# Kernel tuning notes

Measured on AMD Instinct MI355X. Metric: run time of the kernel, lower is better.

The kernel has to match this reference:

```python
import jax, jax.numpy as jnp
import numpy as np

SH_DIM = 9                      # (sh_deg+1)^2, sh_deg=2
DATA_DIM = SH_DIM * 3 + 1       # 28
FINE = 8
COARSE = 32
RADIUS = 1.3
NUM_ATOMS = 16
BATCH = 128
STEP = (RADIUS * 2.0 / COARSE / FINE) / 2.0   # fine_voxel_len / 2
N_INTRS = COARSE * 3 * 2 * FINE               # 1536


def sh_encode(dirs):
    # degree-2 real spherical harmonics bases, [.., 9]
    x, y, z = dirs[..., 0], dirs[..., 1], dirs[..., 2]
    C0 = 0.28209479177387814
    C1 = 0.4886025119029199
    C2 = (1.0925484305920792, -1.0925484305920792, 0.31539156525252005,
          -1.0925484305920792, 0.5462742152960396)
    return jnp.stack([
        jnp.full_like(x, C0), -C1 * y, C1 * z, -C1 * x,
        C2[0] * x * y, C2[1] * y * z, C2[2] * (2.0 * z * z - x * x - y * y),
        C2[3] * x * z, C2[4] * (x * x - y * y)], axis=-1)


def dict_interp(grid, atoms, pts):
    # pts: [N,3] normalized to [0,1). grid: [COARSE^3, A]. atoms: [FINE^3, A, D].
    # coarse voxel -> dictionary coefficients; trilinear interp of atoms inside it.
    cpos = pts * COARSE
    cidx = jnp.clip(jnp.floor(cpos), 0, COARSE - 1)
    ci = cidx.astype(jnp.int32)
    coeff = grid[(ci[:, 0] * COARSE + ci[:, 1]) * COARSE + ci[:, 2]]  # [N, A]
    local = cpos - cidx                       # [0,1) within coarse voxel
    fpos = local * FINE - 0.5
    f0f = jnp.floor(fpos)
    w = fpos - f0f                            # trilinear weights
    f0 = f0f.astype(jnp.int32)
    out = jnp.zeros((pts.shape[0], DATA_DIM), dtype=pts.dtype)
    for dx in (0, 1):
        for dy in (0, 1):
            for dz in (0, 1):
                ix = jnp.clip(f0[:, 0] + dx, 0, FINE - 1)
                iy = jnp.clip(f0[:, 1] + dy, 0, FINE - 1)
                iz = jnp.clip(f0[:, 2] + dz, 0, FINE - 1)
                wt = ((w[:, 0] if dx else 1.0 - w[:, 0]) *
                      (w[:, 1] if dy else 1.0 - w[:, 1]) *
                      (w[:, 2] if dz else 1.0 - w[:, 2]))
                vals = jnp.einsum('na,nad->nd', coeff, atoms[(ix * FINE + iy) * FINE + iz])
                out = out + wt[:, None] * vals
    return out


def setup_inputs() -> dict:
    key = jax.random.key(0)
    k1, k2, k3, k4 = jax.random.split(key, 4)
    rays_o = jnp.array([0.0, 0.0, -2.0 * RADIUS]) + 0.05 * jax.random.normal(k1, (BATCH, 3), jnp.float32)
    d = 0.25 * jax.random.normal(k2, (BATCH, 3), jnp.float32) + jnp.array([0.0, 0.0, 1.0])
    rays_d = d / jnp.linalg.norm(d, axis=-1, keepdims=True)
    grid = 0.01 * jax.random.normal(k3, (COARSE ** 3, NUM_ATOMS), jnp.float32)
    atoms_sh = jax.random.uniform(k4, (FINE ** 3, NUM_ATOMS, DATA_DIM - 1), jnp.float32)
    atoms = jnp.concatenate([atoms_sh, jnp.full((FINE ** 3, NUM_ATOMS, 1), 0.01, jnp.float32)], -1)
    return {"rays_o": rays_o, "rays_d": rays_d, "grid": grid, "atoms": atoms, "grid_id": 0}


def reference(rays_o, rays_d, grid, atoms, grid_id):
    B = rays_o.shape[0]
    # ---- sample_proposal (no-grad in original) ----
    off_pos = (RADIUS - rays_o) / rays_d
    off_neg = (-RADIUS - rays_o) / rays_d
    start = jnp.max(jnp.minimum(off_pos, off_neg), axis=-1, keepdims=True)
    steps = jnp.arange(N_INTRS, dtype=rays_o.dtype)[None, :]
    intersections = jax.lax.stop_gradient(start + steps * STEP)        # [B, 1536]
    tsec = intersections[:, :-1]                                       # [B, M]
    M = N_INTRS - 1
    pts = rays_o[:, None, :] + tsec[:, :, None] * rays_d[:, None, :]   # [B, M, 3]
    mask = jnp.all((pts > -RADIUS) & (pts < RADIUS), axis=-1)          # [B, M]
    pts_n = jnp.clip((pts + RADIUS) / (2.0 * RADIUS), 0.0, 1.0 - 1e-6)
    pts_n = jax.lax.stop_gradient(pts_n).reshape(-1, 3)
    # ---- dictionary interpolation (computed densely, zeroed by mask) ----
    data = dict_interp(grid, atoms, pts_n).reshape(B, M, DATA_DIM)
    sigma = jax.nn.relu(jnp.where(mask, data[..., -1], 0.0))           # [B, M]
    # ---- sigma -> alpha / weights ----
    dists = (intersections[:, 1:] - intersections[:, :-1]) * jnp.linalg.norm(rays_d, axis=-1, keepdims=True)
    alpha = 1.0 - jnp.exp(-sigma * dists)
    trans = jnp.concatenate([jnp.ones((B, 1), alpha.dtype),
                             jnp.cumprod(1.0 - alpha + 1e-10, axis=-1)[:, :-1]], axis=-1)
    abs_light = alpha * trans                                          # [B, M]
    # ---- SH -> rgb, composite ----
    sh_mult = sh_encode(rays_d)[:, None, None, :]                      # [B,1,1,9]
    sh = data[..., :-1].reshape(B, M, 3, SH_DIM)
    rgb_raw = jnp.where(mask[..., None], jnp.sum(sh_mult * sh, axis=-1), 0.0)  # [B,M,3]
    rgb = jnp.sum(abs_light[..., None] * jax.nn.sigmoid(rgb_raw), axis=1)
    rgb = rgb + (1.0 - jnp.sum(abs_light, axis=-1))[:, None]           # white background
    depth = jnp.sum(abs_light * tsec, axis=-1)
    return rgb, alpha, depth
```

## Files before the change

kernel.cpp:

```cpp
#include <hip/hip_runtime.h>
#include <hip/hip_fp16.h>

typedef unsigned int u32;
typedef _Float16 half2v __attribute__((ext_vector_type(2)));
union H2 { u32 u; half2v v; };

#define MSAMP 1535
#define NS 1024
#define RADF 1.3f
#define STEPF ((float)(1.3 * 2.0 / 32.0 / 8.0 / 2.0))

__global__ __launch_bounds__(256) void k_t(const float* __restrict__ atoms,
                                           __half* __restrict__ wst) {
    int o = blockIdx.x * 256 + threadIdx.x;
    int s = o >> 15;
    int r = o & 32767;
    int cell = r >> 6;
    int j = (r >> 4) & 3;
    int a = r & 15;
    wst[o] = __float2half(atoms[(cell * 16 + a) * 28 + s * 4 + j]);
}

__global__ __launch_bounds__(512) void k_p1(const float* __restrict__ ro,
                                            const float* __restrict__ rd,
                                            const float* __restrict__ gridf,
                                            const __half* __restrict__ wst,
                                            __half* __restrict__ raw) {
    __shared__ __half hl[512 * 68];
    int bx = blockIdx.x;
    int s   = bx >> 7;
    int ray = bx & 127;
    int tid = threadIdx.x;

    {
        const uint2* src = (const uint2*)(wst + s * 32768);
#pragma unroll
        for (int it = 0; it < 16; it++) {
            int idx = it * 512 + tid;
            uint2 v = src[idx];
            int cell  = idx >> 4;
            int inner = (idx & 15) << 2;
            *(uint2*)&hl[cell * 68 + inner] = v;
        }
    }
    __syncthreads();

    float ox = ro[ray * 3 + 0], oy = ro[ray * 3 + 1], oz = ro[ray * 3 + 2];
    float dx = rd[ray * 3 + 0], dy = rd[ray * 3 + 1], dz = rd[ray * 3 + 2];
    float a0 = ( RADF - ox) / dx, b0 = (-RADF - ox) / dx;
    float a1 = ( RADF - oy) / dy, b1 = (-RADF - oy) / dy;
    float a2 = ( RADF - oz) / dz, b2 = (-RADF - oz) / dz;
    float st = fmaxf(fmaxf(fminf(a0, b0), fminf(a1, b1)), fminf(a2, b2));

    for (int m = tid; m < NS; m += 512) {
        float t = st + (float)m * STEPF;
        float px = ox + t * dx, py = oy + t * dy, pz = oz + t * dz;
        bool inb = (px > -RADF) && (px < RADF) && (py > -RADF) && (py < RADF)
                && (pz > -RADF) && (pz < RADF);
        if (!inb) continue;

        const float inv2R = 1.0f / 2.6f;
        float pnx = fminf(fmaxf((px + RADF) * inv2R, 0.0f), 0.999999f);
        float pny = fminf(fmaxf((py + RADF) * inv2R, 0.0f), 0.999999f);
        float pnz = fminf(fmaxf((pz + RADF) * inv2R, 0.0f), 0.999999f);

        float cpx = pnx * 32.0f, cpy = pny * 32.0f, cpz = pnz * 32.0f;
        float cfx = floorf(cpx), cfy = floorf(cpy), cfz = floorf(cpz);
        int cix = (int)cfx, ciy = (int)cfy, ciz = (int)cfz;

        float fpx = (cpx - cfx) * 8.0f - 0.5f;
        float fpy = (cpy - cfy) * 8.0f - 0.5f;
        float fpz = (cpz - cfz) * 8.0f - 0.5f;
        float ffx = floorf(fpx), ffy = floorf(fpy), ffz = floorf(fpz);
        int f0x = (int)ffx, f0y = (int)ffy, f0z = (int)ffz;
        float wx = fpx - ffx, wy = fpy - ffy, wz = fpz - ffz;

        int ixa[2] = { max(f0x, 0), min(f0x + 1, 7) };
        int iya[2] = { max(f0y, 0), min(f0y + 1, 7) };
        int iza[2] = { max(f0z, 0), min(f0z + 1, 7) };
        float wxa[2] = { 1.0f - wx, wx };
        float wya[2] = { 1.0f - wy, wy };
        float wza[2] = { 1.0f - wz, wz };

        half2v ch[8];
        {
            const float4* cp = (const float4*)(gridf + (((cix * 32 + ciy) * 32 + ciz) << 4));
            float4 c0 = cp[0], c1 = cp[1], c2 = cp[2], c3 = cp[3];
            ch[0] = half2v{(_Float16)c0.x, (_Float16)c0.y};
            ch[1] = half2v{(_Float16)c0.z, (_Float16)c0.w};
            ch[2] = half2v{(_Float16)c1.x, (_Float16)c1.y};
            ch[3] = half2v{(_Float16)c1.z, (_Float16)c1.w};
            ch[4] = half2v{(_Float16)c2.x, (_Float16)c2.y};
            ch[5] = half2v{(_Float16)c2.z, (_Float16)c2.w};
            ch[6] = half2v{(_Float16)c3.x, (_Float16)c3.y};
            ch[7] = half2v{(_Float16)c3.z, (_Float16)c3.w};
        }

        float acc[4] = {0.0f, 0.0f, 0.0f, 0.0f};

#pragma unroll
        for (int cx = 0; cx < 2; cx++)
#pragma unroll
        for (int cy = 0; cy < 2; cy++)
#pragma unroll
        for (int cz = 0; cz < 2; cz++) {
            float wt = wxa[cx] * wya[cy] * wza[cz];
            int cb = ((ixa[cx] * 8 + iya[cy]) * 8 + iza[cz]) * 68;
            float dd[4] = {0.0f, 0.0f, 0.0f, 0.0f};
#pragma unroll
            for (int g = 0; g < 4; g++) {
#pragma unroll
                for (int j = 0; j < 4; j++) {
                    uint2 q = *(const uint2*)&hl[cb + j * 16 + g * 4];
                    H2 a0h, a1h; a0h.u = q.x; a1h.u = q.y;
                    dd[j] = __builtin_amdgcn_fdot2(a0h.v, ch[2 * g],     dd[j], false);
                    dd[j] = __builtin_amdgcn_fdot2(a1h.v, ch[2 * g + 1], dd[j], false);
                }
            }
#pragma unroll
            for (int j = 0; j < 4; j++) acc[j] = fmaf(wt, dd[j], acc[j]);
        }

        __half2 p0 = __floats2half2_rn(acc[0], acc[1]);
        __half2 p1 = __floats2half2_rn(acc[2], acc[3]);
        uint2 pv;
        pv.x = *(u32*)&p0;
        pv.y = *(u32*)&p1;
        *(uint2*)&raw[(ray * NS + m) * 28 + s * 4] = pv;
    }
}

__global__ __launch_bounds__(512) void k_p2(const float* __restrict__ ro,
                                            const float* __restrict__ rd,
                                            const __half* __restrict__ raw,
                                            float* __restrict__ rgb_out,
                                            float* __restrict__ alpha_out,
                                            float* __restrict__ depth_out) {
    int ray = blockIdx.x;
    int t = threadIdx.x;
    int lane = t & 63, wave = t >> 6;

    int abase = ray * MSAMP;
    for (int m = NS + t; m < MSAMP; m += 512) alpha_out[abase + m] = 0.0f;

    float ox = ro[ray * 3 + 0], oy = ro[ray * 3 + 1], oz = ro[ray * 3 + 2];
    float dx = rd[ray * 3 + 0], dy = rd[ray * 3 + 1], dz = rd[ray * 3 + 2];
    float a0 = ( RADF - ox) / dx, b0 = (-RADF - ox) / dx;
    float a1 = ( RADF - oy) / dy, b1 = (-RADF - oy) / dy;
    float a2 = ( RADF - oz) / dz, b2 = (-RADF - oz) / dz;
    float st = fmaxf(fmaxf(fminf(a0, b0), fminf(a1, b1)), fminf(a2, b2));
    float nrm = sqrtf(dx * dx + dy * dy + dz * dz);

    float shm[9];
    shm[0] = 0.28209479177387814f;
    shm[1] = -0.4886025119029199f * dy;
    shm[2] =  0.4886025119029199f * dz;
    shm[3] = -0.4886025119029199f * dx;
    shm[4] =  1.0925484305920792f * dx * dy;
    shm[5] = -1.0925484305920792f * dy * dz;
    shm[6] =  0.31539156525252005f * (2.0f * dz * dz - dx * dx - dy * dy);
    shm[7] = -1.0925484305920792f * dx * dz;
    shm[8] =  0.5462742152960396f * (dx * dx - dy * dy);

    float av[2], sr[2], sg[2], sb[2];
#pragma unroll
    for (int k = 0; k < 2; k++) {
        int m = t * 2 + k;
        float tm = st + (float)m * STEPF;
        float px = ox + tm * dx, py = oy + tm * dy, pz = oz + tm * dz;
        bool inb = (px > -RADF) && (px < RADF) && (py > -RADF) && (py < RADF)
                && (pz > -RADF) && (pz < RADF);
        float alpha = 0.0f, r0 = 0.0f, r1 = 0.0f, r2 = 0.0f;
        if (inb) {
            const __half* rp = raw + (ray * NS + m) * 28;
            float v[28];
#pragma unroll
            for (int i = 0; i < 7; i++) {
                uint2 q = *(const uint2*)(rp + i * 4);
                __half2 h0 = *(__half2*)&q.x;
                __half2 h1 = *(__half2*)&q.y;
                float2 f0v = __half22float2(h0);
                float2 f1v = __half22float2(h1);
                v[i*4+0] = f0v.x; v[i*4+1] = f0v.y; v[i*4+2] = f1v.x; v[i*4+3] = f1v.y;
            }
            float sigma = fmaxf(v[27], 0.0f);
            alpha = 1.0f - __expf(-sigma * STEPF * nrm);
            float rr[3];
#pragma unroll
            for (int cch = 0; cch < 3; cch++) {
                float sdot = 0.0f;
#pragma unroll
                for (int j = 0; j < 9; j++) sdot = fmaf(shm[j], v[cch * 9 + j], sdot);
                rr[cch] = 1.0f / (1.0f + __expf(-sdot));
            }
            r0 = rr[0]; r1 = rr[1]; r2 = rr[2];
        }
        av[k] = alpha; sr[k] = r0; sg[k] = r1; sb[k] = r2;
        alpha_out[abase + m] = alpha;
    }

    float p = (1.0f - av[0] + 1e-10f) * (1.0f - av[1] + 1e-10f);

    float incl = p;
#pragma unroll
    for (int off = 1; off < 64; off <<= 1) {
        float vv = __shfl_up(incl, off);
        if (lane >= off) incl *= vv;
    }
    __shared__ float wprod[8];
    if (lane == 63) wprod[wave] = incl;
    __syncthreads();
    float excl = __shfl_up(incl, 1);
    if (lane == 0) excl = 1.0f;
    for (int w = 0; w < 8; w++) if (w < wave) excl *= wprod[w];

    float trans = excl;
    float ra = 0.0f, ga = 0.0f, ba = 0.0f, da = 0.0f, wsum = 0.0f;
#pragma unroll
    for (int k = 0; k < 2; k++) {
        int m = t * 2 + k;
        float al = av[k];
        float w = al * trans;
        ra = fmaf(w, sr[k], ra);
        ga = fmaf(w, sg[k], ga);
        ba = fmaf(w, sb[k], ba);
        da = fmaf(w, st + (float)m * STEPF, da);
        wsum += w;
        trans *= (1.0f - al + 1e-10f);
    }

    float vals[5] = { ra, ga, ba, da, wsum };
    __shared__ float wred[8][5];
#pragma unroll
    for (int i = 0; i < 5; i++) {
        float v = vals[i];
        v += __shfl_xor(v, 1);  v += __shfl_xor(v, 2);  v += __shfl_xor(v, 4);
        v += __shfl_xor(v, 8);  v += __shfl_xor(v, 16); v += __shfl_xor(v, 32);
        if (lane == 0) wred[wave][i] = v;
    }
    __syncthreads();
    if (t == 0) {
        float res[5];
#pragma unroll
        for (int i = 0; i < 5; i++) {
            float r_ = 0.0f;
            for (int w = 0; w < 8; w++) r_ += wred[w][i];
            res[i] = r_;
        }
        float omw = 1.0f - res[4];
        rgb_out[ray * 3 + 0] = res[0] + omw;
        rgb_out[ray * 3 + 1] = res[1] + omw;
        rgb_out[ray * 3 + 2] = res[2] + omw;
        depth_out[ray] = res[3];
    }
}

extern "C" void kernel_launch(void* const* d_in, const int* in_sizes, int n_in,
                              void* d_out, int out_size, void* d_ws, size_t ws_size,
                              hipStream_t stream) {
    const float* ro    = (const float*)d_in[0];
    const float* rd    = (const float*)d_in[1];
    const float* grid  = (const float*)d_in[2];
    const float* atoms = (const float*)d_in[3];
    int B = in_sizes[0] / 3;

    __half* wst = (__half*)d_ws;
    __half* raw = (__half*)((char*)d_ws + 458752);

    float* out       = (float*)d_out;
    float* rgb_out   = out;
    float* alpha_out = out + B * 3;
    float* depth_out = out + B * 3 + B * MSAMP;

    hipLaunchKernelGGL(k_t,  dim3(896), dim3(256), 0, stream, atoms, wst);
    hipLaunchKernelGGL(k_p1, dim3(896), dim3(512), 0, stream, ro, rd, grid, wst, raw);
    hipLaunchKernelGGL(k_p2, dim3(B),   dim3(512), 0, stream, ro, rd, raw,
                       rgb_out, alpha_out, depth_out);
}
```

Before: 86.89 us.

## Pack two rays per block in k_p1 and give k_p2 one sample per thread

k_t now reads atoms coalesced and scatters the transposed fp16 writes, instead of gathering strided reads. k_p1 handles two rays per block, so each 64KB shared atom slice is loaded half as often across the grid, and the fill uses 16-byte loads. k_p2 moves to 1024 threads with one sample per thread, which removes the per-thread serial pair and widens the scan to 16 waves. The costs are half as many k_p1 blocks and a larger block for k_p2, which could hurt occupancy or latency hiding.

```diff
diff --git a/kernel.cpp b/kernel.cpp
--- a/kernel.cpp
+++ b/kernel.cpp
@@ -13,12 +13,13 @@
 __global__ __launch_bounds__(256) void k_t(const float* __restrict__ atoms,
                                            __half* __restrict__ wst) {
     int o = blockIdx.x * 256 + threadIdx.x;
-    int s = o >> 15;
-    int r = o & 32767;
-    int cell = r >> 6;
-    int j = (r >> 4) & 3;
-    int a = r & 15;
-    wst[o] = __float2half(atoms[(cell * 16 + a) * 28 + s * 4 + j]);
+    float v = atoms[o];
+    int cell = o / 448;
+    int r = o - cell * 448;
+    int a = r / 28;
+    int d = r - a * 28;
+    int s = d >> 2, j = d & 3;
+    wst[s * 32768 + cell * 64 + j * 16 + a] = __float2half(v);
 }
 
 __global__ __launch_bounds__(512) void k_p1(const float* __restrict__ ro,
@@ -28,19 +29,22 @@
                                             __half* __restrict__ raw) {
     __shared__ __half hl[512 * 68];
     int bx = blockIdx.x;
-    int s   = bx >> 7;
-    int ray = bx & 127;
+    int s  = bx >> 6;
+    int pr = bx & 63;
     int tid = threadIdx.x;
+    int ray = pr * 2 + (tid >> 8);
+    int q   = tid & 255;
 
     {
-        const uint2* src = (const uint2*)(wst + s * 32768);
-#pragma unroll
-        for (int it = 0; it < 16; it++) {
+        const uint4* src = (const uint4*)(wst + s * 32768);
+#pragma unroll
+        for (int it = 0; it < 8; it++) {
             int idx = it * 512 + tid;
-            uint2 v = src[idx];
-            int cell  = idx >> 4;
-            int inner = (idx & 15) << 2;
-            *(uint2*)&hl[cell * 68 + inner] = v;
+            uint4 v = src[idx];
+            int cell  = idx >> 3;
+            int inner = (idx & 7) << 3;
+            *(uint2*)&hl[cell * 68 + inner]     = make_uint2(v.x, v.y);
+            *(uint2*)&hl[cell * 68 + inner + 4] = make_uint2(v.z, v.w);
         }
     }
     __syncthreads();
@@ -52,7 +56,9 @@
     float a2 = ( RADF - oz) / dz, b2 = (-RADF - oz) / dz;
     float st = fmaxf(fmaxf(fminf(a0, b0), fminf(a1, b1)), fminf(a2, b2));
 
-    for (int m = tid; m < NS; m += 512) {
+#pragma unroll
+    for (int k = 0; k < 4; k++) {
+        int m = q + k * 256;
         float t = st + (float)m * STEPF;
         float px = ox + t * dx, py = oy + t * dy, pz = oz + t * dz;
         bool inb = (px > -RADF) && (px < RADF) && (py > -RADF) && (py < RADF)
@@ -111,8 +117,8 @@
             for (int g = 0; g < 4; g++) {
 #pragma unroll
                 for (int j = 0; j < 4; j++) {
-                    uint2 q = *(const uint2*)&hl[cb + j * 16 + g * 4];
-                    H2 a0h, a1h; a0h.u = q.x; a1h.u = q.y;
+                    uint2 qv = *(const uint2*)&hl[cb + j * 16 + g * 4];
+                    H2 a0h, a1h; a0h.u = qv.x; a1h.u = qv.y;
                     dd[j] = __builtin_amdgcn_fdot2(a0h.v, ch[2 * g],     dd[j], false);
                     dd[j] = __builtin_amdgcn_fdot2(a1h.v, ch[2 * g + 1], dd[j], false);
                 }
@@ -130,18 +136,18 @@
     }
 }
 
-__global__ __launch_bounds__(512) void k_p2(const float* __restrict__ ro,
-                                            const float* __restrict__ rd,
-                                            const __half* __restrict__ raw,
-                                            float* __restrict__ rgb_out,
-                                            float* __restrict__ alpha_out,
-                                            float* __restrict__ depth_out) {
+__global__ __launch_bounds__(1024) void k_p2(const float* __restrict__ ro,
+                                             const float* __restrict__ rd,
+                                             const __half* __restrict__ raw,
+                                             float* __restrict__ rgb_out,
+                                             float* __restrict__ alpha_out,
+                                             float* __restrict__ depth_out) {
     int ray = blockIdx.x;
     int t = threadIdx.x;
     int lane = t & 63, wave = t >> 6;
 
     int abase = ray * MSAMP;
-    for (int m = NS + t; m < MSAMP; m += 512) alpha_out[abase + m] = 0.0f;
+    if (NS + t < MSAMP) alpha_out[abase + NS + t] = 0.0f;
 
     float ox = ro[ray * 3 + 0], oy = ro[ray * 3 + 1], oz = ro[ray * 3 + 2];
     float dx = rd[ray * 3 + 0], dy = rd[ray * 3 + 1], dz = rd[ray * 3 + 2];
@@ -162,44 +168,39 @@
     shm[7] = -1.0925484305920792f * dx * dz;
     shm[8] =  0.5462742152960396f * (dx * dx - dy * dy);
 
-    float av[2], sr[2], sg[2], sb[2];
-#pragma unroll
-    for (int k = 0; k < 2; k++) {
-        int m = t * 2 + k;
-        float tm = st + (float)m * STEPF;
-        float px = ox + tm * dx, py = oy + tm * dy, pz = oz + tm * dz;
-        bool inb = (px > -RADF) && (px < RADF) && (py > -RADF) && (py < RADF)
-                && (pz > -RADF) && (pz < RADF);
-        float alpha = 0.0f, r0 = 0.0f, r1 = 0.0f, r2 = 0.0f;
-        if (inb) {
-            const __half* rp = raw + (ray * NS + m) * 28;
-            float v[28];
-#pragma unroll
-            for (int i = 0; i < 7; i++) {
-                uint2 q = *(const uint2*)(rp + i * 4);
-                __half2 h0 = *(__half2*)&q.x;
-                __half2 h1 = *(__half2*)&q.y;
-                float2 f0v = __half22float2(h0);
-                float2 f1v = __half22float2(h1);
-                v[i*4+0] = f0v.x; v[i*4+1] = f0v.y; v[i*4+2] = f1v.x; v[i*4+3] = f1v.y;
-            }
-            float sigma = fmaxf(v[27], 0.0f);
-            alpha = 1.0f - __expf(-sigma * STEPF * nrm);
-            float rr[3];
-#pragma unroll
-            for (int cch = 0; cch < 3; cch++) {
-                float sdot = 0.0f;
-#pragma unroll
-                for (int j = 0; j < 9; j++) sdot = fmaf(shm[j], v[cch * 9 + j], sdot);
-                rr[cch] = 1.0f / (1.0f + __expf(-sdot));
-            }
-            r0 = rr[0]; r1 = rr[1]; r2 = rr[2];
-        }
-        av[k] = alpha; sr[k] = r0; sg[k] = r1; sb[k] = r2;
-        alpha_out[abase + m] = alpha;
-    }
-
-    float p = (1.0f - av[0] + 1e-10f) * (1.0f - av[1] + 1e-10f);
+    int m = t;
+    float tm = st + (float)m * STEPF;
+    float px = ox + tm * dx, py = oy + tm * dy, pz = oz + tm * dz;
+    bool inb = (px > -RADF) && (px < RADF) && (py > -RADF) && (py < RADF)
+            && (pz > -RADF) && (pz < RADF);
+    float alpha = 0.0f, r0 = 0.0f, r1 = 0.0f, r2 = 0.0f;
+    if (inb) {
+        const __half* rp = raw + (ray * NS + m) * 28;
+        float v[28];
+#pragma unroll
+        for (int i = 0; i < 7; i++) {
+            uint2 qv = *(const uint2*)(rp + i * 4);
+            __half2 h0 = *(__half2*)&qv.x;
+            __half2 h1 = *(__half2*)&qv.y;
+            float2 f0v = __half22float2(h0);
+            float2 f1v = __half22float2(h1);
+            v[i*4+0] = f0v.x; v[i*4+1] = f0v.y; v[i*4+2] = f1v.x; v[i*4+3] = f1v.y;
+        }
+        float sigma = fmaxf(v[27], 0.0f);
+        alpha = 1.0f - __expf(-sigma * STEPF * nrm);
+        float rr[3];
+#pragma unroll
+        for (int cch = 0; cch < 3; cch++) {
+            float sdot = 0.0f;
+#pragma unroll
+            for (int j = 0; j < 9; j++) sdot = fmaf(shm[j], v[cch * 9 + j], sdot);
+            rr[cch] = 1.0f / (1.0f + __expf(-sdot));
+        }
+        r0 = rr[0]; r1 = rr[1]; r2 = rr[2];
+    }
+    alpha_out[abase + m] = alpha;
+
+    float p = 1.0f - alpha + 1e-10f;
 
     float incl = p;
 #pragma unroll
@@ -207,30 +208,20 @@
         float vv = __shfl_up(incl, off);
         if (lane >= off) incl *= vv;
     }
-    __shared__ float wprod[8];
+    __shared__ float wprod[16];
     if (lane == 63) wprod[wave] = incl;
     __syncthreads();
     float excl = __shfl_up(incl, 1);
     if (lane == 0) excl = 1.0f;
-    for (int w = 0; w < 8; w++) if (w < wave) excl *= wprod[w];
+    for (int w = 0; w < 16; w++) if (w < wave) excl *= wprod[w];
 
     float trans = excl;
-    float ra = 0.0f, ga = 0.0f, ba = 0.0f, da = 0.0f, wsum = 0.0f;
-#pragma unroll
-    for (int k = 0; k < 2; k++) {
-        int m = t * 2 + k;
-        float al = av[k];
-        float w = al * trans;
-        ra = fmaf(w, sr[k], ra);
-        ga = fmaf(w, sg[k], ga);
-        ba = fmaf(w, sb[k], ba);
-        da = fmaf(w, st + (float)m * STEPF, da);
-        wsum += w;
-        trans *= (1.0f - al + 1e-10f);
-    }
+    float w_ = alpha * trans;
+    float ra = w_ * r0, ga = w_ * r1, ba = w_ * r2;
+    float da = w_ * tm, wsum = w_;
 
     float vals[5] = { ra, ga, ba, da, wsum };
-    __shared__ float wred[8][5];
+    __shared__ float wred[16][5];
 #pragma unroll
     for (int i = 0; i < 5; i++) {
         float v = vals[i];
@@ -244,7 +235,7 @@
 #pragma unroll
         for (int i = 0; i < 5; i++) {
             float r_ = 0.0f;
-            for (int w = 0; w < 8; w++) r_ += wred[w][i];
+            for (int w = 0; w < 16; w++) r_ += wred[w][i];
             res[i] = r_;
         }
         float omw = 1.0f - res[4];
@@ -273,7 +264,7 @@
     float* depth_out = out + B * 3 + B * MSAMP;
 
     hipLaunchKernelGGL(k_t,  dim3(896), dim3(256), 0, stream, atoms, wst);
-    hipLaunchKernelGGL(k_p1, dim3(896), dim3(512), 0, stream, ro, rd, grid, wst, raw);
-    hipLaunchKernelGGL(k_p2, dim3(B),   dim3(512), 0, stream, ro, rd, raw,
+    hipLaunchKernelGGL(k_p1, dim3(448), dim3(512), 0, stream, ro, rd, grid, wst, raw);
+    hipLaunchKernelGGL(k_p2, dim3(B),   dim3(1024), 0, stream, ro, rd, raw,
                        rgb_out, alpha_out, depth_out);
 }
```

Result: no change. 87.58 us (+0.8%).
